# Kernel tuning notes

Measured on AMD Instinct MI355X. Metric: run time of the kernel, lower is better.

The kernel has to match this reference:

```python
import jax, jax.numpy as jnp
import numpy as np
from jax import lax

DIM = 1024
INNER = 2048  # dim * expand_factor
STATE = 64
B, T = 4, 2048
DECAY = 0.95
INPUT_FACTOR = 0.05
LN_EPS = 1e-5


def setup_inputs() -> dict:
    key = jax.random.key(0)
    ks = jax.random.split(key, 8)
    s = 0.02  # small weight scale
    return {
        "x": jax.random.normal(ks[0], (B, T, DIM), jnp.float32),
        "W_in": jax.random.normal(ks[1], (2 * INNER, DIM), jnp.float32) * s,
        "conv_w": jax.random.normal(ks[2], (INNER, 1, 4), jnp.float32) * s,
        "conv_b": jax.random.normal(ks[3], (INNER,), jnp.float32) * s,
        "W_B": jax.random.normal(ks[4], (STATE, INNER), jnp.float32) * s,
        "W_C": jax.random.normal(ks[5], (INNER, STATE), jnp.float32) * s,
        "D_param": jax.random.normal(ks[6], (INNER,), jnp.float32) * s,
        "W_out": jax.random.normal(ks[7], (DIM, INNER), jnp.float32) * s,
        "ln_gamma": jnp.ones((DIM,), jnp.float32),
        "ln_beta": jnp.zeros((DIM,), jnp.float32),
    }


def _layernorm(x, g, b):
    mu = jnp.mean(x, axis=-1, keepdims=True)
    var = jnp.mean(jnp.square(x - mu), axis=-1, keepdims=True)
    return (x - mu) * lax.rsqrt(var + LN_EPS) * g + b


def reference(x, W_in, conv_w, conv_b, W_B, W_C, D_param, W_out, ln_gamma, ln_beta):
    Bn, Tn, Dn = x.shape
    # in_proj -> split into input/gate halves
    x_proj = jnp.einsum("btd,ed->bte", x, W_in)  # [B,T,2*INNER]
    x_input, x_gate = jnp.split(x_proj, 2, axis=-1)
    # depthwise causal conv1d (torch pad=3 then slice [:T] == left-pad 3)
    xc = lax.conv_general_dilated(
        x_input.transpose(0, 2, 1),  # [B,C,T]
        conv_w,                       # [C,1,4]
        window_strides=(1,),
        padding=[(3, 0)],
        feature_group_count=INNER,
    ) + conv_b[None, :, None]
    u = jax.nn.silu(xc).transpose(0, 2, 1)  # [B,T,INNER]
    # linear recurrence: h_t = 0.95*h_{t-1} + 0.05*B_proj(u_t); h_0 = 0
    Bu = jnp.einsum("btc,sc->bts", u, W_B)  # [B,T,STATE]

    def step(h, bu_t):
        h = DECAY * h + INPUT_FACTOR * bu_t
        return h, h

    h0 = jnp.zeros((Bn, STATE), x.dtype)
    _, hs = lax.scan(step, h0, Bu.transpose(1, 0, 2))  # hs: [T,B,STATE]
    hs = hs.transpose(1, 0, 2)  # [B,T,STATE]
    y = jnp.einsum("bts,cs->btc", hs, W_C) + D_param * u  # [B,T,INNER]
    y = y * jax.nn.silu(x_gate)
    y = jnp.einsum("btc,dc->btd", y, W_out)  # [B,T,DIM]
    return _layernorm(y + x, ln_gamma, ln_beta)
```

## Files before the change

kernel.cpp:

```cpp
#include <hip/hip_runtime.h>
#include <hip/hip_bf16.h>

#define T_SEQ 2048
#define DIMD  1024
#define INNER 2048
#define STATE 64
#define BATCH 4
#define NCHUNK 64
#define CHUNK_L (T_SEQ / NCHUNK)
#define MROWS (BATCH * T_SEQ)
#define PSTRIDE ((long)MROWS * STATE)

typedef __hip_bfloat16 bf16;
typedef __attribute__((ext_vector_type(8))) short bf16x8v;
typedef __attribute__((ext_vector_type(4))) float f32x4v;
typedef __attribute__((ext_vector_type(4))) short short4v;

__device__ __forceinline__ float b2f(short s) {
    unsigned u = ((unsigned)(unsigned short)s) << 16;
    float f;
    __builtin_memcpy(&f, &u, 4);
    return f;
}
__device__ __forceinline__ short f2b(float f) {
    bf16 h = __float2bfloat16(f);
    short s;
    __builtin_memcpy(&s, &h, 2);
    return s;
}

__device__ __forceinline__ void gld_lds16(void* lds, const void* gsrc) {
    __builtin_amdgcn_global_load_lds(
        (const __attribute__((address_space(1))) unsigned*)gsrc,
        (__attribute__((address_space(3))) unsigned*)lds, 16, 0, 0);
}

template<int N> __device__ __forceinline__ void waitcnt_vm() {
    if constexpr (N == 8)      asm volatile("s_waitcnt vmcnt(8)" ::: "memory");
    else if constexpr (N == 4) asm volatile("s_waitcnt vmcnt(4)" ::: "memory");
    else                       asm volatile("s_waitcnt vmcnt(0)" ::: "memory");
}
__device__ __forceinline__ void block_barrier() {
    asm volatile("" ::: "memory");
    __builtin_amdgcn_s_barrier();
    asm volatile("" ::: "memory");
}

template<int BM, int BN, int BK, int WR, int WC, int EPI, int SPLITK, int XSWZ>
__global__ __launch_bounds__(WR*WC*64, 2)
void gemm_ring(const short* __restrict__ A, const short* __restrict__ B,
               void* __restrict__ Cout, int M, int N, int K,
               const short* __restrict__ u_ptr, const short* __restrict__ gate_ptr,
               const float* __restrict__ Dp)
{
    constexpr int MFR = BM / (WR * 16);
    constexpr int NFR = BN / (WC * 16);
    constexpr int THREADS = WR * WC * 64;
    constexpr int UPR = BK / 8;
    constexpr int AISS = (BM * UPR) / THREADS;
    constexpr int BISS = (BN * UPR) / THREADS;
    constexpr int LPS  = AISS + BISS;
    __shared__ __align__(16) short As[2][BM * BK];
    __shared__ __align__(16) short Bs[2][BN * BK];

    int bx = blockIdx.x, by = blockIdx.y;
    if constexpr (XSWZ) {
        const int gx = gridDim.x;
        const int nwg = gx * gridDim.y;
        int id = by * gx + bx;
        const int cpx = nwg >> 3;
        id = (id & 7) * cpx + (id >> 3);
        bx = id % gx; by = id / gx;
    }

    const int tid  = threadIdx.x;
    const int lane = tid & 63;
    const int wave = tid >> 6;
    const int wm = (wave / WC) * (MFR * 16);
    const int wn = (wave % WC) * (NFR * 16);
    const long bm = (long)by * BM;
    const long bn = (long)bx * BN;

    f32x4v acc[MFR][NFR];
#pragma unroll
    for (int m = 0; m < MFR; m++)
#pragma unroll
        for (int n = 0; n < NFR; n++)
            acc[m][n] = (f32x4v){0.f, 0.f, 0.f, 0.f};

    const int rsel = lane & 15;
    const int ssrc = (((tid & 7) ^ ((tid >> 3) & 7)) * 8);
    const int swz  = lane & 7;

    int kbeg = 0, kend = K;
    if constexpr (SPLITK > 1) {
        const int kch = K / SPLITK;
        kbeg = blockIdx.z * kch;
        kend = kbeg + kch;
    }
    const int nt = (kend - kbeg) / BK;

    auto stage = [&](int buf, int k0) {
#pragma unroll
        for (int i = 0; i < AISS; i++) {
            const int j = i * THREADS + tid;
            gld_lds16(&As[buf][j * 8],
                      &A[(bm + (j >> 3)) * (long)K + k0 + ssrc]);
        }
#pragma unroll
        for (int i = 0; i < BISS; i++) {
            const int j = i * THREADS + tid;
            gld_lds16(&Bs[buf][j * 8],
                      &B[(bn + (j >> 3)) * (long)K + k0 + ssrc]);
        }
    };
    auto compute = [&](int buf) {
#pragma unroll
        for (int kk = 0; kk < BK; kk += 32) {
            const int slog = (kk >> 3) + (lane >> 4);
            const int soff = ((slog ^ swz) * 8);
            bf16x8v af[MFR], bfv[NFR];
#pragma unroll
            for (int m = 0; m < MFR; m++)
                af[m] = *(const bf16x8v*)&As[buf][(wm + m * 16 + rsel) * BK + soff];
#pragma unroll
            for (int n = 0; n < NFR; n++)
                bfv[n] = *(const bf16x8v*)&Bs[buf][(wn + n * 16 + rsel) * BK + soff];
#pragma unroll
            for (int m = 0; m < MFR; m++)
#pragma unroll
                for (int n = 0; n < NFR; n++)
                    acc[m][n] = __builtin_amdgcn_mfma_f32_16x16x32_bf16(
                        af[m], bfv[n], acc[m][n], 0, 0, 0);
        }
    };

    stage(0, kbeg);
    for (int t = 0; t < nt; ++t) {
        const bool pf = (t + 1 < nt);
        if (pf) stage((t + 1) & 1, kbeg + (t + 1) * BK);
        if (pf) waitcnt_vm<LPS>();
        else    waitcnt_vm<0>();
        block_barrier();
        compute(t & 1);
        block_barrier();
    }

    float* fout = (float*)Cout;
    if constexpr (SPLITK > 1)
        fout += (long)blockIdx.z * (long)M * N;

#pragma unroll
    for (int m = 0; m < MFR; m++) {
#pragma unroll
        for (int n = 0; n < NFR; n++) {
            const long col  = bn + wn + n * 16 + (lane & 15);
            const long row0 = bm + wm + m * 16 + (lane >> 4) * 4;
#pragma unroll
            for (int j = 0; j < 4; j++) {
                const long row = row0 + j;
                const float v = acc[m][n][j];
                const long idx = row * (long)N + col;
                if constexpr (EPI == 0) {
                    ((short*)Cout)[idx] = f2b(v);
                } else if constexpr (EPI == 1) {
                    fout[idx] = v;
                } else if constexpr (EPI == 2) {
                    float uv = b2f(u_ptr[row * (long)INNER + col]);
                    float gv = b2f(gate_ptr[row * (long)(2 * INNER) + col]);
                    float yv = v + Dp[col] * uv;
                    float sg = gv / (1.f + __expf(-gv));
                    ((short*)Cout)[idx] = f2b(yv * sg);
                } else {
                    ((short*)Cout)[idx] = f2b(v + b2f(u_ptr[idx]));
                }
            }
        }
    }
}

__global__ __launch_bounds__(256)
void conv_silu_kernel(const short* __restrict__ xproj, const float* __restrict__ cw,
                      const float* __restrict__ cb, short* __restrict__ u)
{
    const int bt = blockIdx.x;
    const int t  = bt & (T_SEQ - 1);
    const int c0 = threadIdx.x * 8;

    float wreg[4][8];
#pragma unroll
    for (int i = 0; i < 8; i++) {
        float4 wv = *(const float4*)&cw[(c0 + i) * 4];
        wreg[0][i] = wv.x; wreg[1][i] = wv.y; wreg[2][i] = wv.z; wreg[3][i] = wv.w;
    }
    float acc[8];
#pragma unroll
    for (int i = 0; i < 8; i++) acc[i] = cb[c0 + i];

#pragma unroll
    for (int k = 0; k < 4; k++) {
        if (t - 3 + k < 0) continue;
        bf16x8v v = *(const bf16x8v*)&xproj[(long)(bt - 3 + k) * (2 * INNER) + c0];
#pragma unroll
        for (int i = 0; i < 8; i++) acc[i] += b2f(v[i]) * wreg[k][i];
    }
    short o[8];
#pragma unroll
    for (int i = 0; i < 8; i++) {
        float s = acc[i] / (1.f + __expf(-acc[i]));
        o[i] = f2b(s);
    }
    *(bf16x8v*)&u[(long)bt * INNER + c0] = *(const bf16x8v*)o;
}

__global__ __launch_bounds__(64)
void scan_local_kernel(const float* __restrict__ Bu, float* __restrict__ locfin)
{
    const int b  = blockIdx.x / NCHUNK;
    const int ch = blockIdx.x % NCHUNK;
    const long base = ((long)b * T_SEQ + (long)ch * CHUNK_L) * STATE + threadIdx.x;
    float h = 0.f;
#pragma unroll
    for (int t = 0; t < CHUNK_L; t++) {
        const long o = base + (long)t * STATE;
        float bu = (Bu[o] + Bu[o + PSTRIDE]) + (Bu[o + 2 * PSTRIDE] + Bu[o + 3 * PSTRIDE]);
        h = 0.95f * h + 0.05f * bu;
    }
    locfin[(long)blockIdx.x * STATE + threadIdx.x] = h;
}

__global__ __launch_bounds__(256)
void carry_kernel(const float* __restrict__ locfin, float* __restrict__ carry,
                  float decayL)
{
    __shared__ float sm[BATCH * NCHUNK * STATE];
    for (int i = threadIdx.x; i < BATCH * NCHUNK * STATE; i += 256)
        sm[i] = locfin[i];
    __syncthreads();
    const int b = threadIdx.x >> 6, s = threadIdx.x & 63;
    float c = 0.f;
    for (int ch = 0; ch < NCHUNK; ch++) {
        const int idx = (b * NCHUNK + ch) * STATE + s;
        carry[idx] = c;
        c = decayL * c + sm[idx];
    }
}

__global__ __launch_bounds__(64)
void scan_apply_kernel(const float* __restrict__ Bu, const float* __restrict__ carry,
                       short* __restrict__ hs)
{
    const int b  = blockIdx.x / NCHUNK;
    const int ch = blockIdx.x % NCHUNK;
    const long base = ((long)b * T_SEQ + (long)ch * CHUNK_L) * STATE + threadIdx.x;
    float h = carry[(long)blockIdx.x * STATE + threadIdx.x];
#pragma unroll
    for (int t = 0; t < CHUNK_L; t++) {
        const long o = base + (long)t * STATE;
        float bu = (Bu[o] + Bu[o + PSTRIDE]) + (Bu[o + 2 * PSTRIDE] + Bu[o + 3 * PSTRIDE]);
        h = 0.95f * h + 0.05f * bu;
        hs[o] = f2b(h);
    }
}

__global__ __launch_bounds__(256)
void ln_kernel(const short* __restrict__ yx, const float* __restrict__ g,
               const float* __restrict__ b, float* __restrict__ out)
{
    const int row = blockIdx.x;
    const int c   = threadIdx.x * 4;
    const long off = (long)row * DIMD + c;
    const short4v yv = *(const short4v*)&yx[off];
    float s0 = b2f(yv[0]), s1 = b2f(yv[1]), s2 = b2f(yv[2]), s3 = b2f(yv[3]);
    float sum = s0 + s1 + s2 + s3;
    float sq  = s0 * s0 + s1 * s1 + s2 * s2 + s3 * s3;
#pragma unroll
    for (int o = 32; o > 0; o >>= 1) {
        sum += __shfl_down(sum, o);
        sq  += __shfl_down(sq, o);
    }
    __shared__ float rs[4], rq[4];
    const int wave = threadIdx.x >> 6, lane = threadIdx.x & 63;
    if (lane == 0) { rs[wave] = sum; rq[wave] = sq; }
    __syncthreads();
    float tsum = rs[0] + rs[1] + rs[2] + rs[3];
    float tsq  = rq[0] + rq[1] + rq[2] + rq[3];
    float mu  = tsum * (1.f / DIMD);
    float inv = rsqrtf(tsq * (1.f / DIMD) - mu * mu + 1e-5f);
    float4 gv = *(const float4*)&g[c];
    float4 bv = *(const float4*)&b[c];
    float4 ov;
    ov.x = (s0 - mu) * inv * gv.x + bv.x;
    ov.y = (s1 - mu) * inv * gv.y + bv.y;
    ov.z = (s2 - mu) * inv * gv.z + bv.z;
    ov.w = (s3 - mu) * inv * gv.w + bv.w;
    *(float4*)&out[off] = ov;
}

#define C4_X   2097152L
#define C4_W1  (C4_X + 1048576L)
#define C4_WB  (C4_W1 + 32768L)
#define C4_WC  (C4_WB + 32768L)
#define C4_TOT (C4_WC + 524288L)

__global__ __launch_bounds__(256)
void cvt5_kernel(const float* __restrict__ x, const float* __restrict__ w1,
                 const float* __restrict__ wB, const float* __restrict__ wC,
                 const float* __restrict__ wO, short* __restrict__ dst)
{
    const long i = (long)blockIdx.x * 256 + threadIdx.x;
    if (i >= C4_TOT) return;
    const float* s;
    long off;
    if      (i < C4_X)  { s = x;  off = i; }
    else if (i < C4_W1) { s = w1; off = i - C4_X; }
    else if (i < C4_WB) { s = wB; off = i - C4_W1; }
    else if (i < C4_WC) { s = wC; off = i - C4_WB; }
    else                { s = wO; off = i - C4_WC; }
    float4 v = *(const float4*)&s[off * 4];
    short4v o = { f2b(v.x), f2b(v.y), f2b(v.z), f2b(v.w) };
    *(short4v*)&dst[i * 4] = o;
}

extern "C" void kernel_launch(void* const* d_in, const int* in_sizes, int n_in,
                              void* d_out, int out_size, void* d_ws, size_t ws_size,
                              hipStream_t stream)
{
    const float* x     = (const float*)d_in[0];
    const float* W_in  = (const float*)d_in[1];
    const float* cw    = (const float*)d_in[2];
    const float* cb    = (const float*)d_in[3];
    const float* W_B   = (const float*)d_in[4];
    const float* W_C   = (const float*)d_in[5];
    const float* Dp    = (const float*)d_in[6];
    const float* W_out = (const float*)d_in[7];
    const float* ln_g  = (const float*)d_in[8];
    const float* ln_b  = (const float*)d_in[9];

    char* p = (char*)d_ws;
    short* xw    = (short*)(p);
    short* w1    = (short*)(p +  16777216);
    short* wB    = (short*)(p +  25165824);
    short* wC    = (short*)(p +  25427968);
    short* wO    = (short*)(p +  25690112);
    short* xproj = (short*)(p +  29884416);
    short* u     = (short*)(p +  96993280);
    short* hs    = (short*)(p + 132644864);
    short* yg    = u;
    short* yx    = xproj;
    float* BuP    = (float*)(p + 16777216);
    float* locfin = (float*)(p + 25165824);
    float* carry  = (float*)(p + 25231360);

    const int M = MROWS;

    cvt5_kernel<<<(int)((C4_TOT + 255) / 256), 256, 0, stream>>>(
        x, W_in, W_B, W_C, W_out, xw);

    gemm_ring<256, 256, 64, 2, 4, 0, 1, 1><<<dim3(2 * INNER / 256, M / 256), 512, 0, stream>>>(
        xw, w1, xproj, M, 2 * INNER, DIMD, nullptr, nullptr, nullptr);

    conv_silu_kernel<<<M, 256, 0, stream>>>(xproj, cw, cb, u);

    gemm_ring<64, 64, 64, 2, 2, 1, 4, 0><<<dim3(1, M / 64, 4), 256, 0, stream>>>(
        u, wB, BuP, M, STATE, INNER, nullptr, nullptr, nullptr);

    float decayL;
    {
        double dd = 1.0;
        for (int i = 0; i < CHUNK_L; i++) dd *= 0.95;
        decayL = (float)dd;
    }
    scan_local_kernel<<<BATCH * NCHUNK, STATE, 0, stream>>>(BuP, locfin);
    carry_kernel<<<1, 256, 0, stream>>>(locfin, carry, decayL);
    scan_apply_kernel<<<BATCH * NCHUNK, STATE, 0, stream>>>(BuP, carry, hs);

    gemm_ring<128, 128, 64, 2, 2, 2, 1, 1><<<dim3(INNER / 128, M / 128), 256, 0, stream>>>(
        hs, wC, yg, M, INNER, STATE, u, xproj + INNER, Dp);

    gemm_ring<128, 128, 64, 2, 2, 3, 1, 1><<<dim3(DIMD / 128, M / 128), 256, 0, stream>>>(
        yg, wO, yx, M, DIMD, INNER, xw, nullptr, nullptr);

    ln_kernel<<<M, 256, 0, stream>>>(yx, ln_g, ln_b, (float*)d_out);
}
```

Before: 243.7 us.

## Add quadrant-phased 256x256 GEMM with per-phase async LDS staging for in_proj

Introduces a new GEMM kernel for the input projection that splits each 256x256 tile into four 128x128 quadrant phases. Each phase issues the global-to-LDS loads for the matching part of the next K tile, then runs its MFMAs, so loads and compute interleave at finer granularity. It raises wave priority around the MFMA bursts. The cost is a block barrier per phase and a more complex wait-count scheme, which could add synchronisation overhead.

```diff
diff --git a/kernel.cpp b/kernel.cpp
--- a/kernel.cpp
+++ b/kernel.cpp
@@ -36,14 +36,141 @@
 }
 
 template<int N> __device__ __forceinline__ void waitcnt_vm() {
-    if constexpr (N == 8)      asm volatile("s_waitcnt vmcnt(8)" ::: "memory");
-    else if constexpr (N == 4) asm volatile("s_waitcnt vmcnt(4)" ::: "memory");
-    else                       asm volatile("s_waitcnt vmcnt(0)" ::: "memory");
+    if constexpr (N == 16)      asm volatile("s_waitcnt vmcnt(16)" ::: "memory");
+    else if constexpr (N == 8)  asm volatile("s_waitcnt vmcnt(8)" ::: "memory");
+    else if constexpr (N == 4)  asm volatile("s_waitcnt vmcnt(4)" ::: "memory");
+    else                        asm volatile("s_waitcnt vmcnt(0)" ::: "memory");
 }
 __device__ __forceinline__ void block_barrier() {
     asm volatile("" ::: "memory");
     __builtin_amdgcn_s_barrier();
     asm volatile("" ::: "memory");
+}
+
+template<int EPI, int XSWZ>
+__global__ __launch_bounds__(512, 2)
+void gemm_8ph(const short* __restrict__ A, const short* __restrict__ B,
+              void* __restrict__ Cout, int M, int N, int K)
+{
+    __shared__ __align__(16) short As[2][2][128 * 64];
+    __shared__ __align__(16) short Bs[2][2][128 * 64];
+
+    int bx = blockIdx.x, by = blockIdx.y;
+    if constexpr (XSWZ) {
+        const int gx = gridDim.x;
+        const int nwg = gx * gridDim.y;
+        int id = by * gx + bx;
+        const int cpx = nwg >> 3;
+        id = (id & 7) * cpx + (id >> 3);
+        bx = id % gx; by = id / gx;
+    }
+
+    const int tid  = threadIdx.x;
+    const int lane = tid & 63;
+    const int wave = tid >> 6;
+    const int wm2 = (wave >> 2) & 1;
+    const int wn2 = wave & 3;
+    const long bm = (long)by * 256;
+    const long bn = (long)bx * 256;
+
+    const int rsel = lane & 15;
+    const int ssrc = (((tid & 7) ^ ((tid >> 3) & 7)) * 8);
+    const int swz  = lane & 7;
+
+    f32x4v acc[4][4][2];
+#pragma unroll
+    for (int q = 0; q < 4; q++)
+#pragma unroll
+        for (int m = 0; m < 4; m++)
+#pragma unroll
+            for (int n = 0; n < 2; n++)
+                acc[q][m][n] = (f32x4v){0.f, 0.f, 0.f, 0.f};
+
+    const int nt = K / 64;
+
+    auto stage_half = [&](int tt, int h) {
+        const int buf = tt & 1;
+        const int half = h >> 1;
+        const int k0 = tt * 64;
+#pragma unroll
+        for (int i = 0; i < 2; i++) {
+            const int j = i * 512 + tid;
+            if (h & 1)
+                gld_lds16(&Bs[buf][half][j * 8],
+                          &B[(bn + half * 128 + (j >> 3)) * (long)K + k0 + ssrc]);
+            else
+                gld_lds16(&As[buf][half][j * 8],
+                          &A[(bm + half * 128 + (j >> 3)) * (long)K + k0 + ssrc]);
+        }
+    };
+
+    stage_half(0, 0); stage_half(0, 1); stage_half(0, 2); stage_half(0, 3);
+    waitcnt_vm<4>();
+    block_barrier();
+
+    for (int t = 0; t < nt; ++t) {
+        const int buf = t & 1;
+#pragma unroll
+        for (int h = 0; h < 4; ++h) {
+            const int QM[4] = {0, 1, 1, 0};
+            const int QN[4] = {0, 0, 1, 1};
+            const int qm = QM[h], qn = QN[h];
+            bf16x8v af[4][2], bfv[2][2];
+#pragma unroll
+            for (int kkh = 0; kkh < 2; kkh++) {
+                const int slog = kkh * 4 + (lane >> 4);
+                const int soff = ((slog ^ swz) * 8);
+#pragma unroll
+                for (int m = 0; m < 4; m++) {
+                    const int ar = wm2 * 64 + m * 16 + rsel;
+                    af[m][kkh] = *(const bf16x8v*)&As[buf][qm][ar * 64 + soff];
+                }
+#pragma unroll
+                for (int n = 0; n < 2; n++) {
+                    const int br = wn2 * 32 + n * 16 + rsel;
+                    bfv[n][kkh] = *(const bf16x8v*)&Bs[buf][qn][br * 64 + soff];
+                }
+            }
+            if (t + 1 < nt) {
+                stage_half(t + 1, h);
+                waitcnt_vm<4>();
+            } else if (h == 0) {
+                waitcnt_vm<0>();
+            }
+            asm volatile("s_waitcnt lgkmcnt(0)" ::: "memory");
+            __builtin_amdgcn_sched_barrier(0);
+            __builtin_amdgcn_s_setprio(1);
+#pragma unroll
+            for (int kkh = 0; kkh < 2; kkh++)
+#pragma unroll
+                for (int m = 0; m < 4; m++)
+#pragma unroll
+                    for (int n = 0; n < 2; n++)
+                        acc[h][m][n] = __builtin_amdgcn_mfma_f32_16x16x32_bf16(
+                            af[m][kkh], bfv[n][kkh], acc[h][m][n], 0, 0, 0);
+            __builtin_amdgcn_s_setprio(0);
+            block_barrier();
+        }
+    }
+
+#pragma unroll
+    for (int q = 0; q < 4; q++) {
+        const int QM[4] = {0, 1, 1, 0};
+        const int QN[4] = {0, 0, 1, 1};
+#pragma unroll
+        for (int m = 0; m < 4; m++) {
+#pragma unroll
+            for (int n = 0; n < 2; n++) {
+                const long col  = bn + QN[q] * 128 + wn2 * 32 + n * 16 + (lane & 15);
+                const long row0 = bm + QM[q] * 128 + wm2 * 64 + m * 16 + (lane >> 4) * 4;
+#pragma unroll
+                for (int j = 0; j < 4; j++) {
+                    const long idx = (row0 + j) * (long)N + col;
+                    ((short*)Cout)[idx] = f2b(acc[q][m][n][j]);
+                }
+            }
+        }
+    }
 }
 
 template<int BM, int BN, int BK, int WR, int WC, int EPI, int SPLITK, int XSWZ>
@@ -357,8 +484,8 @@
     cvt5_kernel<<<(int)((C4_TOT + 255) / 256), 256, 0, stream>>>(
         x, W_in, W_B, W_C, W_out, xw);
 
-    gemm_ring<256, 256, 64, 2, 4, 0, 1, 1><<<dim3(2 * INNER / 256, M / 256), 512, 0, stream>>>(
-        xw, w1, xproj, M, 2 * INNER, DIMD, nullptr, nullptr, nullptr);
+    gemm_8ph<0, 1><<<dim3(2 * INNER / 256, M / 256), 512, 0, stream>>>(
+        xw, w1, xproj, M, 2 * INNER, DIMD);
 
     conv_silu_kernel<<<M, 256, 0, stream>>>(xproj, cw, cb, u);
 
```

Result: no change. 243.0 us (-0.3%).
